# Performance work log

Measured on AMD Instinct MI355X. Metric: run time of the kernel, lower is better.

## Reference

```python
import jax, jax.numpy as jnp
import numpy as np

B, T, HIN = 4, 2048, 1024
H, E = 16, 64


def setup_inputs() -> dict:
    key = jax.random.key(0)
    k1, k2, k3, k4, k5 = jax.random.split(key, 5)
    s = 1.0 / np.sqrt(HIN)
    return {
        "query": jax.random.normal(k1, (B, T, HIN), dtype=jnp.float32),
        "key_value": jax.random.normal(k2, (B, T, HIN), dtype=jnp.float32),
        "Wq": jax.random.uniform(k3, (HIN, H * E), dtype=jnp.float32, minval=-s, maxval=s),
        "Wk": jax.random.uniform(k4, (HIN, H * E), dtype=jnp.float32, minval=-s, maxval=s),
        "Wv": jax.random.uniform(k5, (HIN, H * E), dtype=jnp.float32, minval=-s, maxval=s),
    }


def reference(query, key_value, Wq, Wk, Wv):
    b, t, _ = query.shape
    scale = E ** (-0.25)  # applied to both q and k, matching e**(1/4) division
    q = (query @ Wq).reshape(b, t, H, E) * scale      # [b,t,h,e]
    k = (key_value @ Wk).reshape(b, t, H, E) * scale  # [b,t,h,e]
    v = (key_value @ Wv).reshape(b, t, H, E)          # [b,t,h,e]
    dot = jnp.einsum("bqhe,bkhe->bhqk", q, k)         # [b,h,t,t]
    attn = jax.nn.softmax(dot, axis=-1)
    out = jnp.einsum("bhqk,bkhe->bqhe", attn, v)      # [b,t,h,e]
    return out.reshape(b, t, H * E)
```

## Files before the change

kernel.cpp:

```cpp
#include <hip/hip_runtime.h>
#include <hip/hip_bf16.h>
#include <stdint.h>


typedef __bf16 bf16;
typedef __attribute__((ext_vector_type(8))) __bf16 bf16x8;
typedef __attribute__((ext_vector_type(4))) __bf16 bf16x4;
typedef __attribute__((ext_vector_type(4))) float f32x4;
typedef __attribute__((ext_vector_type(4))) short s16x4;

#define B_    4
#define T_    2048
#define HIN_  1024
#define H_    16
#define E_    64
#define NOUT_ 1024
#define LOG2E 1.4426950408889634f
#define QKSCALE 0.35355339059327373f
#define QSCALE  (QKSCALE * LOG2E)

__device__ __forceinline__ void gl_lds16(const void* g, void* l) {
  __builtin_amdgcn_global_load_lds((__attribute__((address_space(1))) void*)g,
                                   (__attribute__((address_space(3))) void*)l,
                                   16, 0, 0);
}

__global__ __launch_bounds__(256) void prep_kernel(const float* __restrict__ Xq,
                                                   const float* __restrict__ Xkv,
                                                   const float* __restrict__ Wq,
                                                   const float* __restrict__ Wk,
                                                   const float* __restrict__ Wv,
                                                   bf16* __restrict__ Xb,
                                                   bf16* __restrict__ Wt) {
  __shared__ float s[32][33];
  const int bid = blockIdx.x, tid = threadIdx.x;
  if (bid < 8192) {
    const float* src = (bid < 4096) ? Xq : Xkv;
    bf16* dst = Xb + (size_t)(bid >> 12) * (8192 * 1024);
    size_t i = ((size_t)(bid & 4095) * 256 + tid) * 8;
    float4 f0 = ((const float4*)(src + i))[0];
    float4 f1 = ((const float4*)(src + i))[1];
    bf16x8 t = {(bf16)f0.x, (bf16)f0.y, (bf16)f0.z, (bf16)f0.w,
                (bf16)f1.x, (bf16)f1.y, (bf16)f1.z, (bf16)f1.w};
    *(bf16x8*)(dst + i) = t;
  } else {
    const int wb = bid - 8192;
    const int z = wb >> 10, r = wb & 1023;
    const float* W = (z == 0) ? Wq : ((z == 1) ? Wk : Wv);
    bf16* out = Wt + (size_t)z * HIN_ * NOUT_;
    const int n0 = (r & 31) * 32, k0 = (r >> 5) * 32;
    const int tx = tid & 31, ty = tid >> 5;
#pragma unroll
    for (int i = 0; i < 4; i++)
      s[ty + i * 8][tx] = W[(size_t)(k0 + ty + i * 8) * NOUT_ + n0 + tx];
    __syncthreads();
#pragma unroll
    for (int i = 0; i < 4; i++)
      out[(size_t)(n0 + ty + i * 8) * HIN_ + k0 + tx] = (bf16)s[tx][ty + i * 8];
  }
}

__global__ __launch_bounds__(256, 4) void proj_kernel(const bf16* __restrict__ Xb,
                                                      const bf16* __restrict__ Wt,
                                                      bf16* __restrict__ Qb,
                                                      bf16* __restrict__ Kb,
                                                      bf16* __restrict__ Vtb) {
  __shared__ bf16 As[128 * 64];
  __shared__ bf16 Bs[128 * 64];
  const int z = blockIdx.z;
  const bf16* Abase = (z == 0) ? Xb : ((z == 1) ? Xb + (size_t)8192 * 1024 : Wt + (size_t)2 * HIN_ * NOUT_);
  const bf16* Bbase = (z == 0) ? Wt : ((z == 1) ? Wt + (size_t)HIN_ * NOUT_ : Xb + (size_t)8192 * 1024);
  const int mt = (z == 2) ? blockIdx.y : blockIdx.x;
  const int nt = (z == 2) ? blockIdx.x : blockIdx.y;
  const int m0 = mt * 128, n0 = nt * 128;
  const int tid = threadIdx.x;
  const int w = tid >> 6, lane = tid & 63, quad = lane >> 4, lo = lane & 15;
  const int wm = (w >> 1) * 64, wn = (w & 1) * 64;
  const int srow = w * 8 + (lane >> 3);
  const int schunk = (lane & 7) ^ (srow & 7);

  f32x4 acc[4][4] = {};

  for (int k0 = 0; k0 < HIN_; k0 += 64) {
    __syncthreads();
#pragma unroll
    for (int j = 0; j < 4; j++) {
      int row = j * 32 + srow;
      gl_lds16(Abase + (size_t)(m0 + row) * HIN_ + k0 + schunk * 8, As + (j * 32 + w * 8) * 64);
      gl_lds16(Bbase + (size_t)(n0 + row) * HIN_ + k0 + schunk * 8, Bs + (j * 32 + w * 8) * 64);
    }
    __syncthreads();
#pragma unroll
    for (int kk = 0; kk < 2; kk++) {
      bf16x8 bfrag[4], afrag[4];
#pragma unroll
      for (int j = 0; j < 4; j++) {
        int off = ((((kk << 2) + quad) ^ (lo & 7)) << 3);
        bfrag[j] = *(const bf16x8*)(Bs + (wn + j * 16 + lo) * 64 + off);
        afrag[j] = *(const bf16x8*)(As + (wm + j * 16 + lo) * 64 + off);
      }
#pragma unroll
      for (int i = 0; i < 4; i++)
#pragma unroll
        for (int j = 0; j < 4; j++)
          acc[i][j] = __builtin_amdgcn_mfma_f32_16x16x32_bf16(afrag[i], bfrag[j], acc[i][j], 0, 0, 0);
    }
  }

#pragma unroll
  for (int i = 0; i < 4; i++)
#pragma unroll
    for (int j = 0; j < 4; j++)
#pragma unroll
      for (int r = 0; r < 4; r++) {
        int m = m0 + wm + i * 16 + quad * 4 + r;
        int n = n0 + wn + j * 16 + lo;
        float v = acc[i][j][r];
        if (z == 2) {
          int h = m >> 6, e = m & 63, b = n >> 11, t = n & 2047;
          Vtb[(((size_t)b * H_ + h) * E_ + e) * T_ + t] = (bf16)v;
        } else {
          int b = m >> 11, t = m & 2047, h = n >> 6, e = n & 63;
          if (z == 0)
            Qb[(((size_t)b * H_ + h) * T_ + t) * E_ + e] = (bf16)(v * QSCALE);
          else
            Kb[(((size_t)b * H_ + h) * T_ + t) * E_ + e] = (bf16)(v * QKSCALE);
        }
      }
}

__global__ __launch_bounds__(64, 2) void attn_kernel(const bf16* __restrict__ Qb,
                                                     const bf16* __restrict__ Kb,
                                                     const bf16* __restrict__ Vtb,
                                                     float* __restrict__ out) {
  __shared__ bf16 Vts[2][64 * 64];
  const int lane = threadIdx.x;
  const int quad = lane >> 4, lo = lane & 15;
  const int bh = blockIdx.x, wq = blockIdx.y * 64;
  const bf16* Qg = Qb + (size_t)bh * T_ * E_;
  const bf16* Kg = Kb + (size_t)bh * T_ * E_;
  const bf16* Vg = Vtb + (size_t)bh * E_ * T_;
  const int srow = lane >> 3;
  const int schunk = (lane & 7) ^ (srow & 7);

  bf16x8 qf[4][2];
#pragma unroll
  for (int qi = 0; qi < 4; qi++)
#pragma unroll
    for (int ks = 0; ks < 2; ks++)
      qf[qi][ks] = *(const bf16x8*)(Qg + (size_t)(wq + qi * 16 + lo) * E_ + ks * 32 + quad * 8);

#pragma unroll
  for (int i = 0; i < 8; i++)
    gl_lds16(Vg + (size_t)(i * 8 + srow) * T_ + schunk * 8, &Vts[0][i * 8 * 64]);

  f32x4 acc[4][4] = {};
  float lsum[4] = {0.f, 0.f, 0.f, 0.f};

  for (int kt = 0; kt < 32; kt++) {
    bf16x8 kf[4][2];
#pragma unroll
    for (int ti = 0; ti < 4; ti++)
#pragma unroll
      for (int ks = 0; ks < 2; ks++)
        kf[ti][ks] = *(const bf16x8*)(Kg + (size_t)(kt * 64 + ti * 16 + lo) * E_ + ks * 32 + quad * 8);

    bf16x4 pf[4][4];
#pragma unroll
    for (int qi = 0; qi < 4; qi++) {
      f32x4 st[4] = {};
#pragma unroll
      for (int ks = 0; ks < 2; ks++)
#pragma unroll
        for (int ti = 0; ti < 4; ti++)
          st[ti] = __builtin_amdgcn_mfma_f32_16x16x32_bf16(kf[ti][ks], qf[qi][ks], st[ti], 0, 0, 0);
      float ls = 0.f;
#pragma unroll
      for (int ti = 0; ti < 4; ti++) {
        bf16x4 p4;
#pragma unroll
        for (int r = 0; r < 4; r++) {
          float p = __builtin_amdgcn_exp2f(st[ti][r]);
          ls += p;
          p4[r] = (bf16)p;
        }
        pf[qi][ti] = p4;
      }
      lsum[qi] += ls;
    }

    const bf16* vb = &Vts[kt & 1][0];
#pragma unroll
    for (int tc = 0; tc < 4; tc++)
#pragma unroll
      for (int ej = 0; ej < 4; ej++) {
        bf16x4 vf = *(const bf16x4*)(vb + (ej * 16 + lo) * 64 +
                                     (((tc * 2 + (quad >> 1)) ^ (lo & 7)) << 3) + (quad & 1) * 4);
#pragma unroll
        for (int qi = 0; qi < 4; qi++)
          acc[qi][ej] = __builtin_amdgcn_mfma_f32_16x16x16bf16_1k(
              __builtin_bit_cast(s16x4, pf[qi][tc]), __builtin_bit_cast(s16x4, vf),
              acc[qi][ej], 0, 0, 0);
      }

    const int nt = (kt + 1) & 31;
    bf16* dst = &Vts[(kt + 1) & 1][0];
#pragma unroll
    for (int i = 0; i < 8; i++)
      gl_lds16(Vg + (size_t)(i * 8 + srow) * T_ + nt * 64 + schunk * 8, dst + i * 8 * 64);
  }

  const int b = bh >> 4, h = bh & 15;
#pragma unroll
  for (int qi = 0; qi < 4; qi++) {
    float l = lsum[qi];
    l += __shfl_xor(l, 16);
    l += __shfl_xor(l, 32);
#pragma unroll
    for (int r = 0; r < 4; r++) {
      float linv = __builtin_amdgcn_rcpf(__shfl(l, quad * 4 + r));
      size_t t = wq + qi * 16 + quad * 4 + r;
#pragma unroll
      for (int ej = 0; ej < 4; ej++)
        out[((size_t)b * T_ + t) * NOUT_ + h * E_ + ej * 16 + lo] = acc[qi][ej][r] * linv;
    }
  }
}

extern "C" void kernel_launch(void* const* d_in, const int* in_sizes, int n_in,
                              void* d_out, int out_size, void* d_ws, size_t ws_size,
                              hipStream_t stream) {
  const float* Xq  = (const float*)d_in[0];
  const float* Xkv = (const float*)d_in[1];
  const float* Wq  = (const float*)d_in[2];
  const float* Wk  = (const float*)d_in[3];
  const float* Wv  = (const float*)d_in[4];
  float* out = (float*)d_out;

  char* ws = (char*)d_ws;
  bf16* Qb  = (bf16*)(ws);
  bf16* Kb  = (bf16*)(ws + ((size_t)16 << 20));
  bf16* Vtb = (bf16*)(ws + ((size_t)32 << 20));
  bf16* Wt  = (bf16*)(ws + ((size_t)48 << 20));
  bf16* Xb  = (bf16*)d_out;

  hipLaunchKernelGGL(prep_kernel, dim3(11264), dim3(256), 0, stream, Xq, Xkv, Wq, Wk, Wv, Xb, Wt);
  hipLaunchKernelGGL(proj_kernel, dim3(64, 8, 3), dim3(256), 0, stream, Xb, Wt, Qb, Kb, Vtb);
  hipLaunchKernelGGL(attn_kernel, dim3(64, 32), dim3(64), 0, stream, Qb, Kb, Vtb, out);
}
```

Measured before the change: 268.8 us.

## Share K/V tiles across two waves via LDS in attention kernel

```diff
diff --git a/kernel.cpp b/kernel.cpp
--- a/kernel.cpp
+++ b/kernel.cpp
@@ -129,14 +129,16 @@
       }
 }
 
-__global__ __launch_bounds__(64, 2) void attn_kernel(const bf16* __restrict__ Qb,
-                                                     const bf16* __restrict__ Kb,
-                                                     const bf16* __restrict__ Vtb,
-                                                     float* __restrict__ out) {
+__global__ __launch_bounds__(128, 2) void attn_kernel(const bf16* __restrict__ Qb,
+                                                      const bf16* __restrict__ Kb,
+                                                      const bf16* __restrict__ Vtb,
+                                                      float* __restrict__ out) {
+  __shared__ bf16 Ks[2][64 * 64];
   __shared__ bf16 Vts[2][64 * 64];
-  const int lane = threadIdx.x;
-  const int quad = lane >> 4, lo = lane & 15;
-  const int bh = blockIdx.x, wq = blockIdx.y * 64;
+  const int tid = threadIdx.x;
+  const int w = tid >> 6, lane = tid & 63, quad = lane >> 4, lo = lane & 15;
+  const int bh = blockIdx.x, q0 = blockIdx.y * 128;
+  const int wq = q0 + w * 64;
   const bf16* Qg = Qb + (size_t)bh * T_ * E_;
   const bf16* Kg = Kb + (size_t)bh * T_ * E_;
   const bf16* Vg = Vtb + (size_t)bh * E_ * T_;
@@ -150,64 +152,69 @@
     for (int ks = 0; ks < 2; ks++)
       qf[qi][ks] = *(const bf16x8*)(Qg + (size_t)(wq + qi * 16 + lo) * E_ + ks * 32 + quad * 8);
 
-#pragma unroll
-  for (int i = 0; i < 8; i++)
-    gl_lds16(Vg + (size_t)(i * 8 + srow) * T_ + schunk * 8, &Vts[0][i * 8 * 64]);
-
   f32x4 acc[4][4] = {};
   float lsum[4] = {0.f, 0.f, 0.f, 0.f};
 
-  for (int kt = 0; kt < 32; kt++) {
-    bf16x8 kf[4][2];
-#pragma unroll
-    for (int ti = 0; ti < 4; ti++)
-#pragma unroll
-      for (int ks = 0; ks < 2; ks++)
-        kf[ti][ks] = *(const bf16x8*)(Kg + (size_t)(kt * 64 + ti * 16 + lo) * E_ + ks * 32 + quad * 8);
-
-    bf16x4 pf[4][4];
-#pragma unroll
-    for (int qi = 0; qi < 4; qi++) {
-      f32x4 st[4] = {};
-#pragma unroll
-      for (int ks = 0; ks < 2; ks++)
-#pragma unroll
-        for (int ti = 0; ti < 4; ti++)
-          st[ti] = __builtin_amdgcn_mfma_f32_16x16x32_bf16(kf[ti][ks], qf[qi][ks], st[ti], 0, 0, 0);
-      float ls = 0.f;
-#pragma unroll
-      for (int ti = 0; ti < 4; ti++) {
-        bf16x4 p4;
-#pragma unroll
-        for (int r = 0; r < 4; r++) {
-          float p = __builtin_amdgcn_exp2f(st[ti][r]);
-          ls += p;
-          p4[r] = (bf16)p;
+  for (int kt2 = 0; kt2 < T_ / 128; kt2++) {
+    __syncthreads();
+#pragma unroll
+    for (int sub = 0; sub < 2; sub++) {
+      const int kt = kt2 * 2 + sub;
+#pragma unroll
+      for (int i = 0; i < 4; i++) {
+        int row = w * 32 + i * 8 + srow;
+        gl_lds16(Kg + (size_t)(kt * 64 + row) * E_ + schunk * 8, &Ks[sub][(w * 32 + i * 8) * 64]);
+        gl_lds16(Vg + (size_t)row * T_ + kt * 64 + schunk * 8, &Vts[sub][(w * 32 + i * 8) * 64]);
+      }
+    }
+    __syncthreads();
+
+#pragma unroll
+    for (int sub = 0; sub < 2; sub++) {
+      bf16x8 kf[4][2];
+#pragma unroll
+      for (int ti = 0; ti < 4; ti++)
+#pragma unroll
+        for (int ks = 0; ks < 2; ks++)
+          kf[ti][ks] = *(const bf16x8*)(&Ks[sub][(ti * 16 + lo) * 64 + ((((ks << 2) + quad) ^ (lo & 7)) << 3)]);
+
+      bf16x4 pf[4][4];
+#pragma unroll
+      for (int qi = 0; qi < 4; qi++) {
+        f32x4 st[4] = {};
+#pragma unroll
+        for (int ks = 0; ks < 2; ks++)
+#pragma unroll
+          for (int ti = 0; ti < 4; ti++)
+            st[ti] = __builtin_amdgcn_mfma_f32_16x16x32_bf16(kf[ti][ks], qf[qi][ks], st[ti], 0, 0, 0);
+        float ls = 0.f;
+#pragma unroll
+        for (int ti = 0; ti < 4; ti++) {
+          bf16x4 p4;
+#pragma unroll
+          for (int r = 0; r < 4; r++) {
+            float p = __builtin_amdgcn_exp2f(st[ti][r]);
+            ls += p;
+            p4[r] = (bf16)p;
+          }
+          pf[qi][ti] = p4;
         }
-        pf[qi][ti] = p4;
-      }
-      lsum[qi] += ls;
-    }
-
-    const bf16* vb = &Vts[kt & 1][0];
-#pragma unroll
-    for (int tc = 0; tc < 4; tc++)
-#pragma unroll
-      for (int ej = 0; ej < 4; ej++) {
-        bf16x4 vf = *(const bf16x4*)(vb + (ej * 16 + lo) * 64 +
-                                     (((tc * 2 + (quad >> 1)) ^ (lo & 7)) << 3) + (quad & 1) * 4);
-#pragma unroll
-        for (int qi = 0; qi < 4; qi++)
-          acc[qi][ej] = __builtin_amdgcn_mfma_f32_16x16x16bf16_1k(
-              __builtin_bit_cast(s16x4, pf[qi][tc]), __builtin_bit_cast(s16x4, vf),
-              acc[qi][ej], 0, 0, 0);
-      }
-
-    const int nt = (kt + 1) & 31;
-    bf16* dst = &Vts[(kt + 1) & 1][0];
-#pragma unroll
-    for (int i = 0; i < 8; i++)
-      gl_lds16(Vg + (size_t)(i * 8 + srow) * T_ + nt * 64 + schunk * 8, dst + i * 8 * 64);
+        lsum[qi] += ls;
+      }
+
+#pragma unroll
+      for (int tc = 0; tc < 4; tc++)
+#pragma unroll
+        for (int ej = 0; ej < 4; ej++) {
+          bf16x4 vf = *(const bf16x4*)(&Vts[sub][(ej * 16 + lo) * 64 +
+                                       (((tc * 2 + (quad >> 1)) ^ (lo & 7)) << 3) + (quad & 1) * 4]);
+#pragma unroll
+          for (int qi = 0; qi < 4; qi++)
+            acc[qi][ej] = __builtin_amdgcn_mfma_f32_16x16x16bf16_1k(
+                __builtin_bit_cast(s16x4, pf[qi][tc]), __builtin_bit_cast(s16x4, vf),
+                acc[qi][ej], 0, 0, 0);
+        }
+    }
   }
 
   const int b = bh >> 4, h = bh & 15;
@@ -246,5 +253,5 @@
 
   hipLaunchKernelGGL(prep_kernel, dim3(11264), dim3(256), 0, stream, Xq, Xkv, Wq, Wk, Wv, Xb, Wt);
   hipLaunchKernelGGL(proj_kernel, dim3(64, 8, 3), dim3(256), 0, stream, Xb, Wt, Qb, Kb, Vtb);
-  hipLaunchKernelGGL(attn_kernel, dim3(64, 32), dim3(64), 0, stream, Qb, Kb, Vtb, out);
-}
+  hipLaunchKernelGGL(attn_kernel, dim3(64, 16), dim3(128), 0, stream, Qb, Kb, Vtb, out);
+}
```

New measurement: 288.1 us. 1.07x slower.
